# Performance work log

Measured on AMD Instinct MI355X. Metric: run time of the kernel, lower is better.

## Reference

```python
import jax, jax.numpy as jnp
import numpy as np

B, S, H = 2, 1024, 1024
NH, NKV, HD = 16, 4, 64
F = 2816
E, K = 8, 2
WIN = 256
EPS = 1e-5
THETA = 10000.0


def setup_inputs() -> dict:
    key = jax.random.key(0)
    ks = jax.random.split(key, 13)
    n = lambda k, shp, s=0.02: jax.random.normal(k, shp, jnp.float32) * s
    return dict(
        hidden_states=jax.random.normal(ks[0], (B, S, H), jnp.float32),
        ln1_w=jnp.ones((H,), jnp.float32),
        q_w=n(ks[1], (H, NH * HD)),
        k_w=n(ks[2], (H, NKV * HD)),
        v_w=n(ks[3], (H, NKV * HD)),
        o_w=n(ks[4], (NH * HD, H)),
        res_ln_w=jnp.ones((H,), jnp.float32),
        rw1=n(ks[5], (H, H)),
        rw3=n(ks[6], (H, H)),
        rw2=n(ks[7], (H, H)),
        post_ln_w=jnp.ones((H,), jnp.float32),
        gate_w=n(ks[8], (H, E)),
        e_w1=n(ks[9], (E, H, F)),
        e_w3=n(ks[10], (E, H, F)),
        e_w2=n(ks[11], (E, F, H)),
    )


def _rms(x, w):
    v = jnp.mean(jnp.square(x), -1, keepdims=True)
    return x * jax.lax.rsqrt(v + EPS) * w


def _rope(x):
    # x: [B,S,h,HD]; standard rotate-half RoPE
    pos = jnp.arange(S, dtype=jnp.float32)
    inv = 1.0 / (THETA ** (jnp.arange(0, HD, 2, dtype=jnp.float32) / HD))
    ang = pos[:, None] * inv  # [S, HD/2]
    cos = jnp.concatenate([jnp.cos(ang)] * 2, -1)[None, :, None, :]
    sin = jnp.concatenate([jnp.sin(ang)] * 2, -1)[None, :, None, :]
    x1, x2 = jnp.split(x, 2, axis=-1)
    rot = jnp.concatenate([-x2, x1], -1)
    return x * cos + rot * sin


def _attn(x, q_w, k_w, v_w, o_w):
    q = (x @ q_w).reshape(B, S, NH, HD)
    k = (x @ k_w).reshape(B, S, NKV, HD)
    v = (x @ v_w).reshape(B, S, NKV, HD)
    q, k = _rope(q), _rope(k)
    rep = NH // NKV
    k = jnp.repeat(k, rep, axis=2)
    v = jnp.repeat(v, rep, axis=2)
    sc = jnp.einsum('bqhd,bkhd->bhqk', q, k) * (HD ** -0.5)
    qi = jnp.arange(S)[:, None]
    ki = jnp.arange(S)[None, :]
    mask = (ki <= qi) & (qi - ki < WIN)  # causal sliding window
    sc = jnp.where(mask[None, None], sc, jnp.finfo(sc.dtype).min)
    p = jax.nn.softmax(sc, -1)
    o = jnp.einsum('bhqk,bkhd->bqhd', p, v).reshape(B, S, NH * HD)
    return o @ o_w


def _mlp(x, w1, w3, w2):
    return (jax.nn.silu(x @ w1) * (x @ w3)) @ w2


def _moe(x, gate_w, w1, w3, w2):
    xf = x.reshape(-1, H)  # [T,H]
    T = xf.shape[0]
    logits = xf @ gate_w
    probs = jax.nn.softmax(logits.astype(jnp.float32), -1)
    tw, ti = jax.lax.top_k(probs, K)
    tw = tw / jnp.sum(tw, -1, keepdims=True)
    # combine weights [T,E] via scatter of top-k weights
    cw = jnp.zeros((T, E), jnp.float32).at[jnp.arange(T)[:, None], ti].add(tw)
    h = jax.nn.silu(jnp.einsum('th,ehf->etf', xf, w1)) * jnp.einsum('th,ehf->etf', xf, w3)
    y = jnp.einsum('etf,efh->eth', h, w2)
    out = jnp.einsum('te,eth->th', cw, y)
    return out.reshape(B, S, H)


def reference(hidden_states, ln1_w, q_w, k_w, v_w, o_w, res_ln_w, rw1, rw3, rw2,
              post_ln_w, gate_w, e_w1, e_w3, e_w2):
    residual_input = hidden_states
    h = _rms(hidden_states, ln1_w)
    h = _attn(h, q_w, k_w, v_w, o_w)
    residual_attn = residual_input + h
    # parallel residual dense MLP path (is_residual_mlp=True -> ffn_dim=hidden)
    h = _rms(residual_attn, res_ln_w)
    h = _mlp(h, rw1, rw3, rw2)
    residual_residual = residual_attn + h
    # sparse MoE path operates on the ORIGINAL layer input (Arctic parallel path)
    h = _rms(residual_input, post_ln_w)
    h = _moe(h, gate_w, e_w1, e_w3, e_w2)
    return residual_residual + h
```

## Files before the change

### kernel.cpp

```cpp
#include <hip/hip_runtime.h>
#include <hip/hip_bf16.h>
#include <math.h>

#define B_    2
#define S_    1024
#define H_    1024
#define NH_   16
#define NKV_  4
#define HD_   64
#define F_    2816
#define E_    8
#define WIN_  256
#define T_    (B_*S_)
#define EPS_  1e-5f
#define QKVN_ 1536

typedef __hip_bfloat16 bf16;
using f32x4  = __attribute__((ext_vector_type(4))) float;
using bf16x8 = __attribute__((ext_vector_type(8))) short;

__device__ __forceinline__ float silu_f(float x) { return x / (1.0f + expf(-x)); }

__device__ __forceinline__ unsigned short f2bf(float v) {
  __hip_bfloat16 b = __float2bfloat16(v);
  return *reinterpret_cast<unsigned short*>(&b);
}

__device__ __forceinline__ void stage16(const void* g, void* l) {
#if defined(__has_builtin) && __has_builtin(__builtin_amdgcn_global_load_lds)
  __builtin_amdgcn_global_load_lds((const __attribute__((address_space(1))) unsigned int*)g,
                                   (__attribute__((address_space(3))) unsigned int*)l,
                                   16, 0, 0);
#else
  *(float4*)l = *(const float4*)g;
#endif
}

__global__ void rope_table_kernel(float* __restrict__ costab, float* __restrict__ sintab,
                                  int* __restrict__ counts) {
  int idx = blockIdx.x * blockDim.x + threadIdx.x;
  if (blockIdx.x == 0 && threadIdx.x < E_) counts[threadIdx.x] = 0;
  if (idx >= S_ * 32) return;
  int s = idx >> 5, j = idx & 31;
  float inv = powf(10000.0f, -(float)j / 32.0f);
  float ang = (float)s * inv;
  costab[idx] = cosf(ang);
  sintab[idx] = sinf(ang);
}

__global__ void transpose_cvt_kernel(const float* __restrict__ src, bf16* __restrict__ dst,
                                     int K, int N) {
  __shared__ float tile[32][33];
  const size_t bstride = (size_t)K * N;
  src += bstride * blockIdx.z;
  dst += bstride * blockIdx.z;
  int bk = blockIdx.x * 32, bn = blockIdx.y * 32;
  int tx = threadIdx.x & 31, ty = threadIdx.x >> 5;
  #pragma unroll
  for (int i = 0; i < 4; ++i)
    tile[ty + i * 8][tx] = src[(size_t)(bk + ty + i * 8) * N + bn + tx];
  __syncthreads();
  #pragma unroll
  for (int i = 0; i < 4; ++i)
    dst[(size_t)(bn + ty + i * 8) * K + bk + tx] = __float2bfloat16(tile[tx][ty + i * 8]);
}

struct TransBatch { const float* src[5]; bf16* dst[5]; };
__global__ void transpose_cvt5_kernel(TransBatch tb, int K, int N) {
  __shared__ float tile[32][33];
  const float* src = tb.src[blockIdx.z];
  bf16* dst = tb.dst[blockIdx.z];
  int bk = blockIdx.x * 32, bn = blockIdx.y * 32;
  int tx = threadIdx.x & 31, ty = threadIdx.x >> 5;
  #pragma unroll
  for (int i = 0; i < 4; ++i)
    tile[ty + i * 8][tx] = src[(size_t)(bk + ty + i * 8) * N + bn + tx];
  __syncthreads();
  #pragma unroll
  for (int i = 0; i < 4; ++i)
    dst[(size_t)(bn + ty + i * 8) * K + bk + tx] = __float2bfloat16(tile[tx][ty + i * 8]);
}

__global__ void rms_kernel(const float* __restrict__ x, const float* __restrict__ w,
                           bf16* __restrict__ ob) {
  const int row = blockIdx.x, t = threadIdx.x;
  const float* xr = x + (size_t)row * H_;
  float4 v = *(const float4*)(&xr[t * 4]);
  float ss = v.x*v.x + v.y*v.y + v.z*v.z + v.w*v.w;
  #pragma unroll
  for (int o = 32; o > 0; o >>= 1) ss += __shfl_xor(ss, o);
  __shared__ float red[4];
  if ((t & 63) == 0) red[t >> 6] = ss;
  __syncthreads();
  float tot = red[0] + red[1] + red[2] + red[3];
  float scale = rsqrtf(tot * (1.0f / H_) + EPS_);
  float4 wv = *(const float4*)(&w[t * 4]);
  ushort4 pk = { f2bf(v.x*scale*wv.x), f2bf(v.y*scale*wv.y),
                 f2bf(v.z*scale*wv.z), f2bf(v.w*scale*wv.w) };
  *(ushort4*)((unsigned short*)ob + (size_t)row * H_ + t * 4) = pk;
}

__global__ void rms_gate_kernel(const float* __restrict__ x, const float* __restrict__ w,
                                const float* __restrict__ gw, bf16* __restrict__ ob,
                                int* __restrict__ counts, int* __restrict__ entries,
                                float* __restrict__ wgt) {
  const int row = blockIdx.x, t = threadIdx.x;
  const float* xr = x + (size_t)row * H_;
  float4 v = *(const float4*)(&xr[t * 4]);
  float ss = v.x*v.x + v.y*v.y + v.z*v.z + v.w*v.w;
  #pragma unroll
  for (int o = 32; o > 0; o >>= 1) ss += __shfl_xor(ss, o);
  __shared__ float red[4];
  __shared__ float sm[4][8];
  if ((t & 63) == 0) red[t >> 6] = ss;
  __syncthreads();
  float tot = red[0] + red[1] + red[2] + red[3];
  float scale = rsqrtf(tot * (1.0f / H_) + EPS_);
  float4 wv = *(const float4*)(&w[t * 4]);
  float o0 = v.x*scale*wv.x, o1 = v.y*scale*wv.y, o2 = v.z*scale*wv.z, o3 = v.w*scale*wv.w;
  ushort4 pk = { f2bf(o0), f2bf(o1), f2bf(o2), f2bf(o3) };
  *(ushort4*)((unsigned short*)ob + (size_t)row * H_ + t * 4) = pk;
  const float* gr = gw + (size_t)(t * 4) * E_;
  float acc[E_];
  #pragma unroll
  for (int e = 0; e < E_; ++e)
    acc[e] = o0 * gr[e] + o1 * gr[E_ + e] + o2 * gr[2 * E_ + e] + o3 * gr[3 * E_ + e];
  #pragma unroll
  for (int e = 0; e < E_; ++e) {
    #pragma unroll
    for (int o = 32; o > 0; o >>= 1) acc[e] += __shfl_xor(acc[e], o);
  }
  if ((t & 63) == 0) {
    #pragma unroll
    for (int e = 0; e < E_; ++e) sm[t >> 6][e] = acc[e];
  }
  __syncthreads();
  if (t == 0) {
    float lg[E_];
    #pragma unroll
    for (int e = 0; e < E_; ++e) lg[e] = sm[0][e] + sm[1][e] + sm[2][e] + sm[3][e];
    float m = lg[0];
    #pragma unroll
    for (int e = 1; e < E_; ++e) m = fmaxf(m, lg[e]);
    float p[E_];
    #pragma unroll
    for (int e = 0; e < E_; ++e) p[e] = expf(lg[e] - m);
    int i0 = 0; float b0 = p[0];
    #pragma unroll
    for (int e = 1; e < E_; ++e) if (p[e] > b0) { b0 = p[e]; i0 = e; }
    int i1 = -1; float b1 = -1.f;
    #pragma unroll
    for (int e = 0; e < E_; ++e) if (e != i0 && p[e] > b1) { b1 = p[e]; i1 = e; }
    float inv = 1.f / (b0 + b1);
    wgt[row * 2 + 0] = b0 * inv;
    wgt[row * 2 + 1] = b1 * inv;
    int pos0 = atomicAdd(&counts[i0], 1);
    entries[i0 * T_ + pos0] = row * 2 + 0;
    int pos1 = atomicAdd(&counts[i1], 1);
    entries[i1 * T_ + pos1] = row * 2 + 1;
  }
}

template <int BN, bool ADD_RES>
__global__ __launch_bounds__(256)
void mm_kernel(const bf16* __restrict__ A, const bf16* __restrict__ Bt,
               const float* __restrict__ Res, float* __restrict__ C,
               int M, int N, int K) {
  __shared__ char Al[8192];
  __shared__ char Bl[BN * 64];
  const int t = threadIdx.x;
  const int m0 = blockIdx.y * 128, n0 = blockIdx.x * BN;
  const int lane = t & 63, wid = t >> 6;
  const int wr = wid >> 1, wc = wid & 1;
  const int sr = t >> 2, sc = t & 3;
  const int cA0 = sc ^ ((sr >> 1) & 3);
  const int cA1 = sc ^ (((sr + 64) >> 1) & 3);
  const bf16* gA0 = A + (size_t)(m0 + sr) * K + cA0 * 8;
  const bf16* gA1 = A + (size_t)(m0 + sr + 64) * K + cA1 * 8;
  const bf16* gB0 = Bt + (size_t)(n0 + sr) * K + cA0 * 8;
  const bf16* gB1 = Bt + (size_t)(n0 + sr + 64) * K + cA1 * 8;
  char* lA0 = Al + t * 16;
  char* lA1 = Al + 4096 + t * 16;
  char* lB0 = Bl + t * 16;
  char* lB1 = Bl + 4096 + t * 16;
  const int la = lane & 15, kg = lane >> 4;
  const int swz = (kg ^ ((la >> 1) & 3)) * 16;
  const int aoff = (wr * 64 + la) * 64 + swz;
  constexpr int NW = BN / 32;
  const int boff = (wc * (BN / 2) + la) * 64 + swz;
  f32x4 acc[4][NW] = {};
  for (int k0 = 0; k0 < K; k0 += 32) {
    stage16(gA0 + k0, lA0);
    stage16(gA1 + k0, lA1);
    stage16(gB0 + k0, lB0);
    if constexpr (BN == 128) stage16(gB1 + k0, lB1);
    __syncthreads();
    bf16x8 af[4], bfr[NW];
    #pragma unroll
    for (int i = 0; i < 4; ++i) af[i] = *(const bf16x8*)(Al + aoff + i * 1024);
    #pragma unroll
    for (int i = 0; i < NW; ++i) bfr[i] = *(const bf16x8*)(Bl + boff + i * 1024);
    #pragma unroll
    for (int mi = 0; mi < 4; ++mi)
      #pragma unroll
      for (int ni = 0; ni < NW; ++ni)
        acc[mi][ni] = __builtin_amdgcn_mfma_f32_16x16x32_bf16(af[mi], bfr[ni], acc[mi][ni], 0, 0, 0);
    __syncthreads();
  }
  #pragma unroll
  for (int mi = 0; mi < 4; ++mi) {
    int row = m0 + wr * 64 + mi * 16 + kg * 4;
    #pragma unroll
    for (int ni = 0; ni < NW; ++ni) {
      int col = n0 + wc * (BN / 2) + ni * 16 + la;
      #pragma unroll
      for (int r = 0; r < 4; ++r) {
        size_t off = (size_t)(row + r) * N + col;
        float v = acc[mi][ni][r];
        if (ADD_RES) v += Res[off];
        C[off] = v;
      }
    }
  }
}

__global__ void rope_cvt_qk_kernel(const float* __restrict__ QKV, const float* __restrict__ ct,
                                   const float* __restrict__ st, bf16* __restrict__ Qb,
                                   bf16* __restrict__ Kb) {
  int idx = blockIdx.x * 256 + threadIdx.x;
  int j = idx & 31;
  int hh = (idx >> 5) % 20;
  int t = idx / (32 * 20);
  int s = t & (S_ - 1), b = t >> 10;
  float c = ct[s * 32 + j], sn = st[s * 32 + j];
  if (hh < NH_) {
    const float* src = QKV + (size_t)t * QKVN_ + hh * HD_;
    float x1 = src[j], x2 = src[j + 32];
    bf16* dst = Qb + ((size_t)(b * NH_ + hh) * S_ + s) * HD_;
    dst[j]      = __float2bfloat16((x1 * c - x2 * sn) * 0.125f);
    dst[j + 32] = __float2bfloat16((x2 * c + x1 * sn) * 0.125f);
  } else {
    int kvh = hh - NH_;
    const float* src = QKV + (size_t)t * QKVN_ + 1024 + kvh * HD_;
    float x1 = src[j], x2 = src[j + 32];
    bf16* dst = Kb + ((size_t)(b * NKV_ + kvh) * S_ + s) * HD_;
    dst[j]      = __float2bfloat16(x1 * c - x2 * sn);
    dst[j + 32] = __float2bfloat16(x2 * c + x1 * sn);
  }
}

__global__ void vt_kernel(const float* __restrict__ QKV, bf16* __restrict__ Vt) {
  int p = blockIdx.z;
  int b = p >> 2, kvh = p & 3;
  int s0 = blockIdx.x * 32, d0 = blockIdx.y * 32;
  __shared__ float tile[32][33];
  int tx = threadIdx.x & 31, ty = threadIdx.x >> 5;
  const float* src = QKV + (size_t)(b * S_) * QKVN_ + 1280 + kvh * HD_;
  #pragma unroll
  for (int i = 0; i < 4; ++i)
    tile[ty + i * 8][tx] = src[(size_t)(s0 + ty + i * 8) * QKVN_ + d0 + tx];
  __syncthreads();
  bf16* dst = Vt + (size_t)p * HD_ * S_;
  #pragma unroll
  for (int i = 0; i < 4; ++i)
    dst[(size_t)(d0 + ty + i * 8) * S_ + s0 + tx] = __float2bfloat16(tile[tx][ty + i * 8]);
}

__global__ __launch_bounds__(256)
void attn_kernel(const bf16* __restrict__ Qb, const bf16* __restrict__ Kb,
                 const bf16* __restrict__ Vt, bf16* __restrict__ O) {
  const int w = threadIdx.x >> 6, lane = threadIdx.x & 63;
  const int qw = blockIdx.x * 64 + w * 16;
  const int h = blockIdx.y, b = blockIdx.z, kvh = h >> 2;
  const int g = lane >> 4, qcol = lane & 15;
  const bf16* Qp = Qb + ((size_t)(b * NH_ + h) * S_ + qw) * HD_;
  const bf16* Kp = Kb + (size_t)(b * NKV_ + kvh) * S_ * HD_;
  const bf16* Vp = Vt + (size_t)(b * NKV_ + kvh) * HD_ * S_;
  const bf16x8 qf0 = *(const bf16x8*)(Qp + qcol * HD_ + g * 8);
  const bf16x8 qf1 = *(const bf16x8*)(Qp + qcol * HD_ + 32 + g * 8);
  const int q = qw + qcol;
  float m = -3.0e38f, lsum = 0.f;
  f32x4 o[4] = {};
  int kstart = qw - (WIN_ - 1); if (kstart < 0) kstart = 0; kstart &= ~31;
  const int kend = qw + 16;
  for (int kt = kstart; kt < kend; kt += 32) {
    f32x4 s0 = {}, s1 = {};
    {
      const bf16* kr0 = Kp + (size_t)(kt + qcol) * HD_ + g * 8;
      const bf16* kr1 = kr0 + 16 * HD_;
      bf16x8 kf;
      kf = *(const bf16x8*)(kr0);      s0 = __builtin_amdgcn_mfma_f32_16x16x32_bf16(kf, qf0, s0, 0, 0, 0);
      kf = *(const bf16x8*)(kr0 + 32); s0 = __builtin_amdgcn_mfma_f32_16x16x32_bf16(kf, qf1, s0, 0, 0, 0);
      kf = *(const bf16x8*)(kr1);      s1 = __builtin_amdgcn_mfma_f32_16x16x32_bf16(kf, qf0, s1, 0, 0, 0);
      kf = *(const bf16x8*)(kr1 + 32); s1 = __builtin_amdgcn_mfma_f32_16x16x32_bf16(kf, qf1, s1, 0, 0, 0);
    }
    bool v0[4], v1[4];
    float pmax = -3.0e38f;
    #pragma unroll
    for (int r = 0; r < 4; ++r) {
      int k0r = kt + 4 * g + r;
      int k1r = k0r + 16;
      v0[r] = (k0r <= q) && (q - k0r < WIN_);
      v1[r] = (k1r <= q) && (q - k1r < WIN_);
      s0[r] = v0[r] ? s0[r] : -3.0e38f;
      s1[r] = v1[r] ? s1[r] : -3.0e38f;
      pmax = fmaxf(pmax, fmaxf(s0[r], s1[r]));
    }
    pmax = fmaxf(pmax, __shfl_xor(pmax, 16));
    pmax = fmaxf(pmax, __shfl_xor(pmax, 32));
    const float mnew = fmaxf(m, pmax);
    const float scale = __expf(m - mnew);
    float p0[4], p1[4], psum = 0.f;
    #pragma unroll
    for (int r = 0; r < 4; ++r) {
      p0[r] = v0[r] ? __expf(s0[r] - mnew) : 0.f;
      p1[r] = v1[r] ? __expf(s1[r] - mnew) : 0.f;
      psum += p0[r] + p1[r];
    }
    lsum = lsum * scale + psum;
    #pragma unroll
    for (int df = 0; df < 4; ++df) {
      o[df][0] *= scale; o[df][1] *= scale; o[df][2] *= scale; o[df][3] *= scale;
    }
    m = mnew;
    unsigned pk[4];
    #pragma unroll
    for (int r = 0; r < 4; ++r) pk[r] = (unsigned)f2bf(p0[r]) | ((unsigned)f2bf(p1[r]) << 16);
    const int srcLo = ((g & 1) << 1) * 16 + qcol;
    unsigned lo[4], hi[4];
    #pragma unroll
    for (int r = 0; r < 4; ++r) {
      lo[r] = (unsigned)__shfl((int)pk[r], srcLo);
      hi[r] = (unsigned)__shfl((int)pk[r], srcLo + 16);
    }
    const bool useHi = (g >= 2);
    union { unsigned u[4]; bf16x8 v; } bp;
    {
      unsigned e0 = useHi ? (lo[0] >> 16) : (lo[0] & 0xffffu);
      unsigned e1 = useHi ? (lo[1] >> 16) : (lo[1] & 0xffffu);
      unsigned e2 = useHi ? (lo[2] >> 16) : (lo[2] & 0xffffu);
      unsigned e3 = useHi ? (lo[3] >> 16) : (lo[3] & 0xffffu);
      unsigned e4 = useHi ? (hi[0] >> 16) : (hi[0] & 0xffffu);
      unsigned e5 = useHi ? (hi[1] >> 16) : (hi[1] & 0xffffu);
      unsigned e6 = useHi ? (hi[2] >> 16) : (hi[2] & 0xffffu);
      unsigned e7 = useHi ? (hi[3] >> 16) : (hi[3] & 0xffffu);
      bp.u[0] = e0 | (e1 << 16);
      bp.u[1] = e2 | (e3 << 16);
      bp.u[2] = e4 | (e5 << 16);
      bp.u[3] = e6 | (e7 << 16);
    }
    #pragma unroll
    for (int df = 0; df < 4; ++df) {
      bf16x8 vf = *(const bf16x8*)(Vp + (size_t)(16 * df + qcol) * S_ + kt + g * 8);
      o[df] = __builtin_amdgcn_mfma_f32_16x16x32_bf16(vf, bp.v, o[df], 0, 0, 0);
    }
  }
  lsum += __shfl_xor(lsum, 16);
  lsum += __shfl_xor(lsum, 32);
  const float inv = 1.f / lsum;
  bf16* Op = O + (size_t)(b * S_ + q) * (NH_ * HD_) + h * HD_;
  #pragma unroll
  for (int df = 0; df < 4; ++df) {
    ushort4 st = { f2bf(o[df][0] * inv), f2bf(o[df][1] * inv),
                   f2bf(o[df][2] * inv), f2bf(o[df][3] * inv) };
    *(ushort4*)((unsigned short*)Op + 16 * df + 4 * g) = st;
  }
}

__global__ void silu_mul_kernel(const float* __restrict__ GU, unsigned short* __restrict__ out) {
  int idx = blockIdx.x * 256 + threadIdx.x;
  int tok = idx >> 8, c = idx & 255;
  const float4 gv = *(const float4*)(GU + (size_t)tok * 2048 + c * 4);
  const float4 uv = *(const float4*)(GU + (size_t)tok * 2048 + 1024 + c * 4);
  ushort4 pk = { f2bf(silu_f(gv.x) * uv.x), f2bf(silu_f(gv.y) * uv.y),
                 f2bf(silu_f(gv.z) * uv.z), f2bf(silu_f(gv.w) * uv.w) };
  *(ushort4*)(out + (size_t)tok * 1024 + c * 4) = pk;
}

__global__ __launch_bounds__(256)
void moe_ffn1_kernel(const bf16* __restrict__ X, const bf16* __restrict__ W1t,
                     const bf16* __restrict__ W3t,
                     const int* __restrict__ counts, const int* __restrict__ entries,
                     bf16* __restrict__ Hb) {
  const int e = blockIdx.z;
  const int n_e = counts[e];
  const int r0 = blockIdx.y * 128;
  if (r0 >= n_e) return;
  const int f0 = blockIdx.x * 128;
  __shared__ char Al[8192], B1l[8192], B3l[8192];
  __shared__ int rowent[128];
  const int t = threadIdx.x;
  if (t < 128) { int r = r0 + t; rowent[t] = (r < n_e) ? entries[e * T_ + r] : -1; }
  __syncthreads();
  const int lane = t & 63, wid = t >> 6, wr = wid >> 1, wc = wid & 1;
  const int sr = t >> 2, sc = t & 3;
  const int c0 = sc ^ ((sr >> 1) & 3);
  const int c1 = sc ^ (((sr + 64) >> 1) & 3);
  int ea = rowent[sr], eb = rowent[sr + 64];
  const bf16* gA0 = X + (size_t)(ea < 0 ? 0 : (ea >> 1)) * H_ + c0 * 8;
  const bf16* gA1 = X + (size_t)(eb < 0 ? 0 : (eb >> 1)) * H_ + c1 * 8;
  const bf16* W1b = W1t + (size_t)e * F_ * H_;
  const bf16* W3b = W3t + (size_t)e * F_ * H_;
  const bf16* gB10 = W1b + (size_t)(f0 + sr) * H_ + c0 * 8;
  const bf16* gB11 = W1b + (size_t)(f0 + sr + 64) * H_ + c1 * 8;
  const bf16* gB30 = W3b + (size_t)(f0 + sr) * H_ + c0 * 8;
  const bf16* gB31 = W3b + (size_t)(f0 + sr + 64) * H_ + c1 * 8;
  char* lA0 = Al + t * 16;   char* lA1 = Al + 4096 + t * 16;
  char* l10 = B1l + t * 16;  char* l11 = B1l + 4096 + t * 16;
  char* l30 = B3l + t * 16;  char* l31 = B3l + 4096 + t * 16;
  const int la = lane & 15, kg = lane >> 4;
  const int swz = (kg ^ ((la >> 1) & 3)) * 16;
  const int aoff = (wr * 64 + la) * 64 + swz;
  const int boff = (wc * 64 + la) * 64 + swz;
  f32x4 acc1[4][4] = {}, acc3[4][4] = {};
  for (int k0 = 0; k0 < H_; k0 += 32) {
    stage16(gA0 + k0, lA0);
    stage16(gA1 + k0, lA1);
    stage16(gB10 + k0, l10);
    stage16(gB11 + k0, l11);
    stage16(gB30 + k0, l30);
    stage16(gB31 + k0, l31);
    __syncthreads();
    bf16x8 af[4], b1f[4], b3f[4];
    #pragma unroll
    for (int i = 0; i < 4; ++i) af[i] = *(const bf16x8*)(Al + aoff + i * 1024);
    #pragma unroll
    for (int i = 0; i < 4; ++i) b1f[i] = *(const bf16x8*)(B1l + boff + i * 1024);
    #pragma unroll
    for (int i = 0; i < 4; ++i) b3f[i] = *(const bf16x8*)(B3l + boff + i * 1024);
    #pragma unroll
    for (int mi = 0; mi < 4; ++mi)
      #pragma unroll
      for (int ni = 0; ni < 4; ++ni) {
        acc1[mi][ni] = __builtin_amdgcn_mfma_f32_16x16x32_bf16(af[mi], b1f[ni], acc1[mi][ni], 0, 0, 0);
        acc3[mi][ni] = __builtin_amdgcn_mfma_f32_16x16x32_bf16(af[mi], b3f[ni], acc3[mi][ni], 0, 0, 0);
      }
    __syncthreads();
  }
  #pragma unroll
  for (int mi = 0; mi < 4; ++mi) {
    int rloc = wr * 64 + mi * 16 + kg * 4;
    #pragma unroll
    for (int ni = 0; ni < 4; ++ni) {
      int col = f0 + wc * 64 + ni * 16 + la;
      #pragma unroll
      for (int r = 0; r < 4; ++r) {
        int ent = rowent[rloc + r];
        if (ent < 0) continue;
        float gv = acc1[mi][ni][r], uv = acc3[mi][ni][r];
        Hb[(size_t)ent * F_ + col] = __float2bfloat16(silu_f(gv) * uv);
      }
    }
  }
}

__global__ __launch_bounds__(256)
void moe_ffn2_kernel(const bf16* __restrict__ Hb, const bf16* __restrict__ W2t,
                     const int* __restrict__ counts, const int* __restrict__ entries,
                     float* __restrict__ Y) {
  const int e = blockIdx.z;
  const int n_e = counts[e];
  const int r0 = blockIdx.y * 128;
  if (r0 >= n_e) return;
  const int n0 = blockIdx.x * 128;
  __shared__ char Al[8192], Bl[8192];
  __shared__ int rowent[128];
  const int t = threadIdx.x;
  if (t < 128) { int r = r0 + t; rowent[t] = (r < n_e) ? entries[e * T_ + r] : -1; }
  __syncthreads();
  const int lane = t & 63, wid = t >> 6, wr = wid >> 1, wc = wid & 1;
  const int sr = t >> 2, sc = t & 3;
  const int c0 = sc ^ ((sr >> 1) & 3);
  const int c1 = sc ^ (((sr + 64) >> 1) & 3);
  int ea = rowent[sr], eb = rowent[sr + 64];
  const bf16* gA0 = Hb + (size_t)(ea < 0 ? 0 : ea) * F_ + c0 * 8;
  const bf16* gA1 = Hb + (size_t)(eb < 0 ? 0 : eb) * F_ + c1 * 8;
  const bf16* W2b = W2t + (size_t)e * H_ * F_;
  const bf16* gB0 = W2b + (size_t)(n0 + sr) * F_ + c0 * 8;
  const bf16* gB1 = W2b + (size_t)(n0 + sr + 64) * F_ + c1 * 8;
  char* lA0 = Al + t * 16;  char* lA1 = Al + 4096 + t * 16;
  char* lB0 = Bl + t * 16;  char* lB1 = Bl + 4096 + t * 16;
  const int la = lane & 15, kg = lane >> 4;
  const int swz = (kg ^ ((la >> 1) & 3)) * 16;
  const int aoff = (wr * 64 + la) * 64 + swz;
  const int boff = (wc * 64 + la) * 64 + swz;
  f32x4 acc[4][4] = {};
  for (int k0 = 0; k0 < F_; k0 += 32) {
    stage16(gA0 + k0, lA0);
    stage16(gA1 + k0, lA1);
    stage16(gB0 + k0, lB0);
    stage16(gB1 + k0, lB1);
    __syncthreads();
    bf16x8 af[4], bfr[4];
    #pragma unroll
    for (int i = 0; i < 4; ++i) af[i] = *(const bf16x8*)(Al + aoff + i * 1024);
    #pragma unroll
    for (int i = 0; i < 4; ++i) bfr[i] = *(const bf16x8*)(Bl + boff + i * 1024);
    #pragma unroll
    for (int mi = 0; mi < 4; ++mi)
      #pragma unroll
      for (int ni = 0; ni < 4; ++ni)
        acc[mi][ni] = __builtin_amdgcn_mfma_f32_16x16x32_bf16(af[mi], bfr[ni], acc[mi][ni], 0, 0, 0);
    __syncthreads();
  }
  #pragma unroll
  for (int mi = 0; mi < 4; ++mi) {
    int rloc = wr * 64 + mi * 16 + kg * 4;
    #pragma unroll
    for (int ni = 0; ni < 4; ++ni) {
      int col = n0 + wc * 64 + ni * 16 + la;
      #pragma unroll
      for (int r = 0; r < 4; ++r) {
        int ent = rowent[rloc + r];
        if (ent < 0) continue;
        Y[(size_t)ent * H_ + col] = acc[mi][ni][r];
      }
    }
  }
}

__global__ void combine_kernel(const float* __restrict__ Y, const float* __restrict__ wgt,
                               float* __restrict__ out) {
  int t = blockIdx.x;
  int c = threadIdx.x;
  float w0 = wgt[t * 2], w1 = wgt[t * 2 + 1];
  float4 y0 = *(const float4*)(&Y[((size_t)t * 2) * H_ + c * 4]);
  float4 y1 = *(const float4*)(&Y[((size_t)t * 2 + 1) * H_ + c * 4]);
  float4 o  = *(float4*)(&out[(size_t)t * H_ + c * 4]);
  o.x += w0 * y0.x + w1 * y1.x;
  o.y += w0 * y0.y + w1 * y1.y;
  o.z += w0 * y0.z + w1 * y1.z;
  o.w += w0 * y0.w + w1 * y1.w;
  *(float4*)(&out[(size_t)t * H_ + c * 4]) = o;
}

extern "C" void kernel_launch(void* const* d_in, const int* in_sizes, int n_in,
                              void* d_out, int out_size, void* d_ws, size_t ws_size,
                              hipStream_t stream) {
  const float* hidden    = (const float*)d_in[0];
  const float* ln1_w     = (const float*)d_in[1];
  const float* q_w       = (const float*)d_in[2];
  const float* k_w       = (const float*)d_in[3];
  const float* v_w       = (const float*)d_in[4];
  const float* o_w       = (const float*)d_in[5];
  const float* res_ln_w  = (const float*)d_in[6];
  const float* rw1       = (const float*)d_in[7];
  const float* rw3       = (const float*)d_in[8];
  const float* rw2       = (const float*)d_in[9];
  const float* post_ln_w = (const float*)d_in[10];
  const float* gate_w    = (const float*)d_in[11];
  const float* e_w1      = (const float*)d_in[12];
  const float* e_w3      = (const float*)d_in[13];
  const float* e_w2      = (const float*)d_in[14];
  float* out = (float*)d_out;

  char* base = (char*)d_ws;
  size_t off = 0;
  auto alloc = [&](size_t bytes) -> void* {
    void* p = base + off;
    off += (bytes + 255) & ~(size_t)255;
    return p;
  };
  float* qkvf   = (float*)alloc((size_t)T_ * QKVN_ * 4);
  float* costab = (float*)alloc((size_t)S_ * 32 * 4);
  float* sintab = (float*)alloc((size_t)S_ * 32 * 4);
  float* resat  = (float*)alloc((size_t)T_ * H_ * 4);
  float* gu     = (float*)alloc((size_t)T_ * 2048 * 4);
  float* wgt    = (float*)alloc((size_t)T_ * 2 * 4);
  float* Y      = (float*)alloc((size_t)T_ * 2 * H_ * 4);
  bf16* h1b     = (bf16*)alloc((size_t)T_ * H_ * 2);
  bf16* h2b     = (bf16*)alloc((size_t)T_ * H_ * 2);
  bf16* h3b     = (bf16*)alloc((size_t)T_ * H_ * 2);
  bf16* attnb   = (bf16*)alloc((size_t)T_ * H_ * 2);
  bf16* gb      = (bf16*)alloc((size_t)T_ * H_ * 2);
  bf16* Hb      = (bf16*)alloc((size_t)T_ * 2 * F_ * 2);
  bf16* Qbuf    = (bf16*)alloc((size_t)B_ * NH_ * S_ * HD_ * 2);
  bf16* Kbuf    = (bf16*)alloc((size_t)B_ * NKV_ * S_ * HD_ * 2);
  bf16* Vtbuf   = (bf16*)alloc((size_t)B_ * NKV_ * HD_ * S_ * 2);
  bf16* qkvwt   = (bf16*)alloc((size_t)QKVN_ * H_ * 2);
  bf16* owt     = (bf16*)alloc((size_t)H_ * H_ * 2);
  bf16* w13t    = (bf16*)alloc((size_t)2048 * H_ * 2);
  bf16* rw2t    = (bf16*)alloc((size_t)H_ * H_ * 2);
  bf16* ew1t    = (bf16*)alloc((size_t)E_ * F_ * H_ * 2);
  bf16* ew3t    = (bf16*)alloc((size_t)E_ * F_ * H_ * 2);
  bf16* ew2t    = (bf16*)alloc((size_t)E_ * H_ * F_ * 2);
  int* counts   = (int*)alloc(64);
  int* entries  = (int*)alloc((size_t)E_ * T_ * 4);

  rope_table_kernel<<<(S_ * 32 + 255) / 256, 256, 0, stream>>>(costab, sintab, counts);

  {
    TransBatch tb;
    tb.src[0] = q_w;  tb.dst[0] = qkvwt;
    tb.src[1] = o_w;  tb.dst[1] = owt;
    tb.src[2] = rw1;  tb.dst[2] = w13t;
    tb.src[3] = rw3;  tb.dst[3] = w13t + (size_t)1024 * 1024;
    tb.src[4] = rw2;  tb.dst[4] = rw2t;
    transpose_cvt5_kernel<<<dim3(32, 32, 5), 256, 0, stream>>>(tb, 1024, 1024);
  }
  {
    TransBatch tb = {};
    tb.src[0] = k_w;  tb.dst[0] = qkvwt + (size_t)1024 * 1024;
    tb.src[1] = v_w;  tb.dst[1] = qkvwt + (size_t)1280 * 1024;
    transpose_cvt5_kernel<<<dim3(32, 8, 2), 256, 0, stream>>>(tb, 1024, 256);
  }
  transpose_cvt_kernel<<<dim3(32, 88, 8), 256, 0, stream>>>(e_w1, ew1t, 1024, 2816);
  transpose_cvt_kernel<<<dim3(32, 88, 8), 256, 0, stream>>>(e_w3, ew3t, 1024, 2816);
  transpose_cvt_kernel<<<dim3(88, 32, 8), 256, 0, stream>>>(e_w2, ew2t, 2816, 1024);

  rms_kernel<<<T_, 256, 0, stream>>>(hidden, ln1_w, h1b);
  mm_kernel<64, false><<<dim3(QKVN_ / 64, T_ / 128), 256, 0, stream>>>(h1b, qkvwt, nullptr, qkvf, T_, QKVN_, H_);
  rope_cvt_qk_kernel<<<(T_ * 20 * 32) / 256, 256, 0, stream>>>(qkvf, costab, sintab, Qbuf, Kbuf);
  vt_kernel<<<dim3(32, 2, 8), 256, 0, stream>>>(qkvf, Vtbuf);
  attn_kernel<<<dim3(S_ / 64, NH_, B_), 256, 0, stream>>>(Qbuf, Kbuf, Vtbuf, attnb);
  mm_kernel<64, true><<<dim3(16, 16), 256, 0, stream>>>(attnb, owt, hidden, resat, T_, H_, H_);

  rms_kernel<<<T_, 256, 0, stream>>>(resat, res_ln_w, h2b);
  mm_kernel<128, false><<<dim3(16, 16), 256, 0, stream>>>(h2b, w13t, nullptr, gu, T_, 2048, H_);
  silu_mul_kernel<<<T_, 256, 0, stream>>>(gu, (unsigned short*)gb);
  mm_kernel<64, true><<<dim3(16, 16), 256, 0, stream>>>(gb, rw2t, resat, out, T_, H_, H_);

  rms_gate_kernel<<<T_, 256, 0, stream>>>(hidden, post_ln_w, gate_w, h3b, counts, entries, wgt);
  moe_ffn1_kernel<<<dim3(F_ / 128, 16, E_), 256, 0, stream>>>(h3b, ew1t, ew3t, counts, entries, Hb);
  moe_ffn2_kernel<<<dim3(8, 16, E_), 256, 0, stream>>>(Hb, ew2t, counts, entries, Y);
  combine_kernel<<<T_, 256, 0, stream>>>(Y, wgt, out);
}
```

Baseline: 775.2 us.

## Double-buffer LDS tiles in dense and MoE GEMM kernels to overlap loads

Gives the shared-memory A/B tiles in mm_kernel, moe_ffn1_kernel and moe_ffn2_kernel two buffers. The next K-slice is prefetched into the alternate buffer while MFMAs consume the current one, and the barrier that used to sit between staging and compute is dropped. The aim is to hide global-memory latency behind matrix math. The cost is double the LDS footprint (48 KB in ffn1), which can lower occupancy, and correctness relies on the end-of-iteration barrier also waiting for outstanding staged loads.

Result: faster. 749.3 us (-3.3%).

```diff
diff --git a/kernel.cpp b/kernel.cpp
--- a/kernel.cpp
+++ b/kernel.cpp
@@ -166,8 +166,8 @@
 void mm_kernel(const bf16* __restrict__ A, const bf16* __restrict__ Bt,
                const float* __restrict__ Res, float* __restrict__ C,
                int M, int N, int K) {
-  __shared__ char Al[8192];
-  __shared__ char Bl[BN * 64];
+  __shared__ char Al[2][8192];
+  __shared__ char Bl[2][BN * 64];
   const int t = threadIdx.x;
   const int m0 = blockIdx.y * 128, n0 = blockIdx.x * BN;
   const int lane = t & 63, wid = t >> 6;
@@ -179,27 +179,28 @@
   const bf16* gA1 = A + (size_t)(m0 + sr + 64) * K + cA1 * 8;
   const bf16* gB0 = Bt + (size_t)(n0 + sr) * K + cA0 * 8;
   const bf16* gB1 = Bt + (size_t)(n0 + sr + 64) * K + cA1 * 8;
-  char* lA0 = Al + t * 16;
-  char* lA1 = Al + 4096 + t * 16;
-  char* lB0 = Bl + t * 16;
-  char* lB1 = Bl + 4096 + t * 16;
   const int la = lane & 15, kg = lane >> 4;
   const int swz = (kg ^ ((la >> 1) & 3)) * 16;
   const int aoff = (wr * 64 + la) * 64 + swz;
   constexpr int NW = BN / 32;
   const int boff = (wc * (BN / 2) + la) * 64 + swz;
+  auto STAGE = [&](int buf, int k0) {
+    stage16(gA0 + k0, Al[buf] + t * 16);
+    stage16(gA1 + k0, Al[buf] + 4096 + t * 16);
+    stage16(gB0 + k0, Bl[buf] + t * 16);
+    if constexpr (BN == 128) stage16(gB1 + k0, Bl[buf] + 4096 + t * 16);
+  };
   f32x4 acc[4][NW] = {};
+  STAGE(0, 0);
+  __syncthreads();
   for (int k0 = 0; k0 < K; k0 += 32) {
-    stage16(gA0 + k0, lA0);
-    stage16(gA1 + k0, lA1);
-    stage16(gB0 + k0, lB0);
-    if constexpr (BN == 128) stage16(gB1 + k0, lB1);
-    __syncthreads();
+    const int cur = (k0 >> 5) & 1;
+    if (k0 + 32 < K) STAGE(cur ^ 1, k0 + 32);
     bf16x8 af[4], bfr[NW];
     #pragma unroll
-    for (int i = 0; i < 4; ++i) af[i] = *(const bf16x8*)(Al + aoff + i * 1024);
-    #pragma unroll
-    for (int i = 0; i < NW; ++i) bfr[i] = *(const bf16x8*)(Bl + boff + i * 1024);
+    for (int i = 0; i < 4; ++i) af[i] = *(const bf16x8*)(Al[cur] + aoff + i * 1024);
+    #pragma unroll
+    for (int i = 0; i < NW; ++i) bfr[i] = *(const bf16x8*)(Bl[cur] + boff + i * 1024);
     #pragma unroll
     for (int mi = 0; mi < 4; ++mi)
       #pragma unroll
@@ -387,7 +388,7 @@
   const int r0 = blockIdx.y * 128;
   if (r0 >= n_e) return;
   const int f0 = blockIdx.x * 128;
-  __shared__ char Al[8192], B1l[8192], B3l[8192];
+  __shared__ char Al[2][8192], B1l[2][8192], B3l[2][8192];
   __shared__ int rowent[128];
   const int t = threadIdx.x;
   if (t < 128) { int r = r0 + t; rowent[t] = (r < n_e) ? entries[e * T_ + r] : -1; }
@@ -405,29 +406,31 @@
   const bf16* gB11 = W1b + (size_t)(f0 + sr + 64) * H_ + c1 * 8;
   const bf16* gB30 = W3b + (size_t)(f0 + sr) * H_ + c0 * 8;
   const bf16* gB31 = W3b + (size_t)(f0 + sr + 64) * H_ + c1 * 8;
-  char* lA0 = Al + t * 16;   char* lA1 = Al + 4096 + t * 16;
-  char* l10 = B1l + t * 16;  char* l11 = B1l + 4096 + t * 16;
-  char* l30 = B3l + t * 16;  char* l31 = B3l + 4096 + t * 16;
   const int la = lane & 15, kg = lane >> 4;
   const int swz = (kg ^ ((la >> 1) & 3)) * 16;
   const int aoff = (wr * 64 + la) * 64 + swz;
   const int boff = (wc * 64 + la) * 64 + swz;
+  auto STAGE = [&](int buf, int k0) {
+    stage16(gA0 + k0, Al[buf] + t * 16);
+    stage16(gA1 + k0, Al[buf] + 4096 + t * 16);
+    stage16(gB10 + k0, B1l[buf] + t * 16);
+    stage16(gB11 + k0, B1l[buf] + 4096 + t * 16);
+    stage16(gB30 + k0, B3l[buf] + t * 16);
+    stage16(gB31 + k0, B3l[buf] + 4096 + t * 16);
+  };
   f32x4 acc1[4][4] = {}, acc3[4][4] = {};
+  STAGE(0, 0);
+  __syncthreads();
   for (int k0 = 0; k0 < H_; k0 += 32) {
-    stage16(gA0 + k0, lA0);
-    stage16(gA1 + k0, lA1);
-    stage16(gB10 + k0, l10);
-    stage16(gB11 + k0, l11);
-    stage16(gB30 + k0, l30);
-    stage16(gB31 + k0, l31);
-    __syncthreads();
+    const int cur = (k0 >> 5) & 1;
+    if (k0 + 32 < H_) STAGE(cur ^ 1, k0 + 32);
     bf16x8 af[4], b1f[4], b3f[4];
     #pragma unroll
-    for (int i = 0; i < 4; ++i) af[i] = *(const bf16x8*)(Al + aoff + i * 1024);
-    #pragma unroll
-    for (int i = 0; i < 4; ++i) b1f[i] = *(const bf16x8*)(B1l + boff + i * 1024);
-    #pragma unroll
-    for (int i = 0; i < 4; ++i) b3f[i] = *(const bf16x8*)(B3l + boff + i * 1024);
+    for (int i = 0; i < 4; ++i) af[i] = *(const bf16x8*)(Al[cur] + aoff + i * 1024);
+    #pragma unroll
+    for (int i = 0; i < 4; ++i) b1f[i] = *(const bf16x8*)(B1l[cur] + boff + i * 1024);
+    #pragma unroll
+    for (int i = 0; i < 4; ++i) b3f[i] = *(const bf16x8*)(B3l[cur] + boff + i * 1024);
     #pragma unroll
     for (int mi = 0; mi < 4; ++mi)
       #pragma unroll
@@ -463,7 +466,7 @@
   const int r0 = blockIdx.y * 128;
   if (r0 >= n_e) return;
   const int n0 = blockIdx.x * 128;
-  __shared__ char Al[8192], Bl[8192];
+  __shared__ char Al[2][8192], Bl[2][8192];
   __shared__ int rowent[128];
   const int t = threadIdx.x;
   if (t < 128) { int r = r0 + t; rowent[t] = (r < n_e) ? entries[e * T_ + r] : -1; }
@@ -478,24 +481,27 @@
   const bf16* W2b = W2t + (size_t)e * H_ * F_;
   const bf16* gB0 = W2b + (size_t)(n0 + sr) * F_ + c0 * 8;
   const bf16* gB1 = W2b + (size_t)(n0 + sr + 64) * F_ + c1 * 8;
-  char* lA0 = Al + t * 16;  char* lA1 = Al + 4096 + t * 16;
-  char* lB0 = Bl + t * 16;  char* lB1 = Bl + 4096 + t * 16;
   const int la = lane & 15, kg = lane >> 4;
   const int swz = (kg ^ ((la >> 1) & 3)) * 16;
   const int aoff = (wr * 64 + la) * 64 + swz;
   const int boff = (wc * 64 + la) * 64 + swz;
+  auto STAGE = [&](int buf, int k0) {
+    stage16(gA0 + k0, Al[buf] + t * 16);
+    stage16(gA1 + k0, Al[buf] + 4096 + t * 16);
+    stage16(gB0 + k0, Bl[buf] + t * 16);
+    stage16(gB1 + k0, Bl[buf] + 4096 + t * 16);
+  };
   f32x4 acc[4][4] = {};
+  STAGE(0, 0);
+  __syncthreads();
   for (int k0 = 0; k0 < F_; k0 += 32) {
-    stage16(gA0 + k0, lA0);
-    stage16(gA1 + k0, lA1);
-    stage16(gB0 + k0, lB0);
-    stage16(gB1 + k0, lB1);
-    __syncthreads();
+    const int cur = (k0 >> 5) & 1;
+    if (k0 + 32 < F_) STAGE(cur ^ 1, k0 + 32);
     bf16x8 af[4], bfr[4];
     #pragma unroll
-    for (int i = 0; i < 4; ++i) af[i] = *(const bf16x8*)(Al + aoff + i * 1024);
-    #pragma unroll
-    for (int i = 0; i < 4; ++i) bfr[i] = *(const bf16x8*)(Bl + boff + i * 1024);
+    for (int i = 0; i < 4; ++i) af[i] = *(const bf16x8*)(Al[cur] + aoff + i * 1024);
+    #pragma unroll
+    for (int i = 0; i < 4; ++i) bfr[i] = *(const bf16x8*)(Bl[cur] + boff + i * 1024);
     #pragma unroll
     for (int mi = 0; mi < 4; ++mi)
       #pragma unroll
```
